# Kernel tuning notes

Hardware: AMD Instinct MI355X
Metric: run time of the kernel (lower is better)

## Reference

```python
import jax, jax.numpy as jnp
import numpy as np

EMBED = 8      # embed_dim == n_qubits == d_k (forced by reshapes in the source)
FFN = 2048
LN_EPS = 1e-5


def _layernorm(x, g, b):
    mu = jnp.mean(x, axis=-1, keepdims=True)
    var = jnp.mean(jnp.square(x - mu), axis=-1, keepdims=True)
    return (x - mu) * jax.lax.rsqrt(var + LN_EPS) * g + b


def _quantum_measure(theta):
    # RX(theta_i) on each wire of |0..0>, CNOT ladder 0->1->...->n-1,
    # then <Z_i>. Closed form: <Z_i> = prod_{j<=i} cos(theta_j).
    return jnp.cumprod(jnp.cos(theta), axis=-1)


def setup_inputs() -> dict:
    key = jax.random.key(0)
    ks = jax.random.split(key, 8)
    B, S = 32, 4096
    s_e = 1.0 / np.sqrt(EMBED)
    s_f = 1.0 / np.sqrt(FFN)
    return {
        "x": jax.random.normal(ks[0], (B, S, EMBED), jnp.float32),
        "Wq": jax.random.uniform(ks[1], (EMBED, EMBED), jnp.float32, -s_e, s_e),
        "Wo": jax.random.uniform(ks[2], (EMBED, EMBED), jnp.float32, -s_e, s_e),
        "W1": jax.random.uniform(ks[3], (FFN, EMBED), jnp.float32, -s_e, s_e),
        "b1": jax.random.uniform(ks[4], (FFN,), jnp.float32, -s_e, s_e),
        "W2": jax.random.uniform(ks[5], (EMBED, FFN), jnp.float32, -s_f, s_f),
        "b2": jax.random.uniform(ks[6], (EMBED,), jnp.float32, -s_f, s_f),
        "g1": jnp.ones((EMBED,), jnp.float32),
        "beta1": jnp.zeros((EMBED,), jnp.float32),
        "g2": jnp.ones((EMBED,), jnp.float32),
        "beta2": jnp.zeros((EMBED,), jnp.float32),
    }


def reference(x, Wq, Wo, W1, b1, W2, b2, g1, beta1, g2, beta2):
    # Quantum multi-head attention (num_heads=1, d_k=n_wires=8).
    # Note: k_proj / v_proj outputs are unused in the original forward.
    q = jnp.einsum("bse,fe->bsf", x, Wq)          # (B,S,E)
    attn = jnp.einsum("bse,fe->bsf", _quantum_measure(q), Wo)
    h = _layernorm(x + attn, g1, beta1)           # dropout is identity (eval)
    # Quantum feed-forward: measure -> linear1 -> relu -> linear2
    m = _quantum_measure(h)                       # (B,S,E)
    hid = jax.nn.relu(jnp.einsum("bse,fe->bsf", m, W1) + b1)  # (B,S,FFN)
    ffn = jnp.einsum("bsf,ef->bse", hid, W2) + b2
    return _layernorm(h + ffn, g2, beta2)
```

## Files before the change

kernel.cpp:

```cpp
#include <hip/hip_runtime.h>
#include <hip/hip_bf16.h>

#define FFN 2048
#define LN_EPS 1e-5f

typedef __attribute__((ext_vector_type(8))) short bf16x8;
typedef __attribute__((ext_vector_type(4))) float f32x4;

union FragU { bf16x8 v; unsigned u[4]; uint4 q; };

static __device__ __forceinline__ unsigned cvtpk(float lo, float hi) {
    unsigned r;
    asm("v_cvt_pk_bf16_f32 %0, %1, %2" : "=v"(r) : "v"(lo), "v"(hi));
    return r;
}

static __device__ __forceinline__ unsigned pkrelu(unsigned a, unsigned z) {
    unsigned r;
    asm("v_pk_max_f16 %0, %1, %2" : "=v"(r) : "v"(a), "v"(z));
    return r;
}

static __device__ __forceinline__ ushort to_bf16(float f) {
    unsigned u = __float_as_uint(f);
    u += 0x7fffu + ((u >> 16) & 1u);
    return (ushort)(u >> 16);
}

__global__ __launch_bounds__(256) void tbq_prep(
    const float* __restrict__ W1, const float* __restrict__ b1,
    const float* __restrict__ W2, uint4* __restrict__ ws)
{
    const int idx = blockIdx.x * 256 + threadIdx.x;
    if (idx >= 6336) return;
    ushort v[8] = {0,0,0,0,0,0,0,0};
    if (idx < 4224) {
        const int rec = idx / 33, r = idx % 33;
        if (r) {
            const int l32 = r - 1, c = l32 & 15, g = l32 >> 4;
            const int s = rec & 1, cc = rec >> 1;
            const int f = cc * 32 + s * 16 + c;
            if (g == 0) {
                #pragma unroll
                for (int j = 0; j < 8; ++j) v[j] = to_bf16(W1[f * 8 + j]);
            } else {
                v[0] = to_bf16(b1[f]);
            }
        }
    } else {
        const int i2 = idx - 4224;
        const int rec = i2 / 33, r = i2 % 33;
        if (r) {
            const int l32 = r - 1, g = l32 >> 3, c = l32 & 7, cc = rec;
            #pragma unroll
            for (int j = 0; j < 8; ++j) {
                const int fl = 4 * g + (j & 3) + 16 * (j >> 2);
                v[j] = to_bf16(W2[c * FFN + cc * 32 + fl]);
            }
        }
    }
    union { ushort s[8]; uint4 q; } pk;
    #pragma unroll
    for (int j = 0; j < 8; ++j) pk.s[j] = v[j];
    ws[idx] = pk.q;
}

__global__ __launch_bounds__(256) void tbq_mfma(
    const float* __restrict__ x,
    const float* __restrict__ Wq,
    const float* __restrict__ Wo,
    const float* __restrict__ b2,
    const float* __restrict__ g1,
    const float* __restrict__ beta1,
    const float* __restrict__ g2,
    const float* __restrict__ beta2,
    const uint4* __restrict__ ws,
    float* __restrict__ out)
{
    __shared__ __align__(16) uint4 mS[128];
    __shared__ __align__(16) float part[4][128][8];

    const int tid  = threadIdx.x;
    const int lane = tid & 63;
    const int wv   = tid >> 6;
    const int c    = lane & 15;
    const int g    = lane >> 4;
    const int tok0 = blockIdx.x * 128;

    const int o1 = (lane < 32) ? (1 + lane) : 0;
    const int o2 = ((lane & 8) == 0) ? (1 + ((lane >> 4) << 3) + (lane & 7)) : 0;

    float h[8];
    if (tid < 128) {
        const int t = tok0 + tid;
        const float4* xr = (const float4*)(x + (size_t)t * 8);
        float4 xa = xr[0], xb = xr[1];
        float xv[8] = {xa.x, xa.y, xa.z, xa.w, xb.x, xb.y, xb.z, xb.w};

        float qm[8];
        {
            float cp = 1.0f;
            #pragma unroll
            for (int f = 0; f < 8; ++f) {
                float acc = 0.0f;
                #pragma unroll
                for (int e = 0; e < 8; ++e) acc += xv[e] * Wq[f * 8 + e];
                cp *= __cosf(acc);
                qm[f] = cp;
            }
        }
        float mu = 0.0f;
        #pragma unroll
        for (int f = 0; f < 8; ++f) {
            float acc = 0.0f;
            #pragma unroll
            for (int e = 0; e < 8; ++e) acc += qm[e] * Wo[f * 8 + e];
            h[f] = xv[f] + acc;
            mu += h[f];
        }
        mu *= 0.125f;
        float var = 0.0f;
        #pragma unroll
        for (int i = 0; i < 8; ++i) { float d = h[i] - mu; var += d * d; }
        var *= 0.125f;
        float rs = rsqrtf(var + LN_EPS);
        #pragma unroll
        for (int i = 0; i < 8; ++i) h[i] = (h[i] - mu) * rs * g1[i] + beta1[i];

        float m[8];
        {
            float cp = 1.0f;
            #pragma unroll
            for (int i = 0; i < 8; ++i) { cp *= __cosf(h[i]); m[i] = cp; }
        }
        uint4 mq;
        mq.x = cvtpk(m[0], m[1]); mq.y = cvtpk(m[2], m[3]);
        mq.z = cvtpk(m[4], m[5]); mq.w = cvtpk(m[6], m[7]);
        mS[tid] = mq;
    }
    __syncthreads();

    FragU B1[8];
    #pragma unroll
    for (int T = 0; T < 8; ++T) {
        uint4 mr = mS[T * 16 + c];
        B1[T].u[0] = (g == 0) ? mr.x : ((g == 1) ? 0x00003F80u : 0u);
        B1[T].u[1] = (g == 0) ? mr.y : 0u;
        B1[T].u[2] = (g == 0) ? mr.z : 0u;
        B1[T].u[3] = (g == 0) ? mr.w : 0u;
    }

    f32x4 z4 = {0.f, 0.f, 0.f, 0.f};
    asm volatile("" : "+v"(z4));
    unsigned zz = 0u;
    asm volatile("" : "+v"(zz));

    f32x4 acc[8] = {{0,0,0,0},{0,0,0,0},{0,0,0,0},{0,0,0,0},
                    {0,0,0,0},{0,0,0,0},{0,0,0,0},{0,0,0,0}};
    const int cc0 = wv * 16;

    #pragma unroll 4
    for (int i = 0; i < 16; ++i) {
        const int cc = cc0 + i;
        const uint4* r0 = ws + cc * 66;
        const uint4* r1 = r0 + 33;
        const uint4* r2 = ws + 4224 + cc * 33;
        FragU F0, F1, A2;
        F0.q = r0[o1];
        F1.q = r1[o1];
        A2.q = r2[o2];

        #pragma unroll
        for (int T = 0; T < 8; ++T) {
            f32x4 c0 = __builtin_amdgcn_mfma_f32_16x16x32_bf16(F0.v, B1[T].v, z4, 0, 0, 0);
            f32x4 c1 = __builtin_amdgcn_mfma_f32_16x16x32_bf16(F1.v, B1[T].v, z4, 0, 0, 0);
            FragU B2;
            B2.u[0] = pkrelu(cvtpk(c0[0], c0[1]), zz);
            B2.u[1] = pkrelu(cvtpk(c0[2], c0[3]), zz);
            B2.u[2] = pkrelu(cvtpk(c1[0], c1[1]), zz);
            B2.u[3] = pkrelu(cvtpk(c1[2], c1[3]), zz);
            acc[T] = __builtin_amdgcn_mfma_f32_16x16x32_bf16(A2.v, B2.v, acc[T], 0, 0, 0);
        }
    }

    if (g < 2) {
        #pragma unroll
        for (int T = 0; T < 8; ++T) {
            *(f32x4*)&part[wv][T * 16 + c][4 * g] = acc[T];
        }
    }
    __syncthreads();

    if (tid < 128) {
        float ffnv[8];
        #pragma unroll
        for (int e = 0; e < 8; ++e)
            ffnv[e] = part[0][tid][e] + part[1][tid][e]
                    + part[2][tid][e] + part[3][tid][e];

        float o[8];
        float mu2 = 0.0f;
        #pragma unroll
        for (int i = 0; i < 8; ++i) { o[i] = h[i] + ffnv[i] + b2[i]; mu2 += o[i]; }
        mu2 *= 0.125f;
        float v2 = 0.0f;
        #pragma unroll
        for (int i = 0; i < 8; ++i) { float d = o[i] - mu2; v2 += d * d; }
        v2 *= 0.125f;
        float rs2 = rsqrtf(v2 + LN_EPS);

        float res[8];
        #pragma unroll
        for (int i = 0; i < 8; ++i) res[i] = (o[i] - mu2) * rs2 * g2[i] + beta2[i];

        float4* orow = (float4*)(out + (size_t)(tok0 + tid) * 8);
        orow[0] = make_float4(res[0], res[1], res[2], res[3]);
        orow[1] = make_float4(res[4], res[5], res[6], res[7]);
    }
}

extern "C" void kernel_launch(void* const* d_in, const int* in_sizes, int n_in,
                              void* d_out, int out_size, void* d_ws, size_t ws_size,
                              hipStream_t stream) {
    const float* x     = (const float*)d_in[0];
    const float* Wq    = (const float*)d_in[1];
    const float* Wo    = (const float*)d_in[2];
    const float* W1    = (const float*)d_in[3];
    const float* b1    = (const float*)d_in[4];
    const float* W2    = (const float*)d_in[5];
    const float* b2    = (const float*)d_in[6];
    const float* g1    = (const float*)d_in[7];
    const float* beta1 = (const float*)d_in[8];
    const float* g2    = (const float*)d_in[9];
    const float* beta2 = (const float*)d_in[10];
    float* out = (float*)d_out;
    uint4* ws = (uint4*)d_ws;

    tbq_prep<<<25, 256, 0, stream>>>(W1, b1, W2, ws);

    const int ntok = in_sizes[0] / 8;
    const int grid = ntok / 128;
    tbq_mfma<<<grid, 256, 0, stream>>>(x, Wq, Wo, b2, g1, beta1, g2, beta2, ws, out);
}
```

Before: 37.80 us.

## Prefetch weight fragments three iterations ahead and raise wave priority around MFMAs

The FFN loop now software-pipelines the weight fragment loads into a 4-slot register ring. The first three chunks are issued before the prologue's attention/LayerNorm math, so those loads overlap with it, and each later load is issued three iterations early. The MFMA block is wrapped in s_setprio raises, and the packed ReLU uses an inline zero constant instead of a zero register. This aims to hide global-load latency on the weights, at the cost of extra VGPRs that may reduce occupancy.

```diff
diff --git a/kernel.cpp b/kernel.cpp
--- a/kernel.cpp
+++ b/kernel.cpp
@@ -15,9 +15,9 @@
     return r;
 }
 
-static __device__ __forceinline__ unsigned pkrelu(unsigned a, unsigned z) {
+static __device__ __forceinline__ unsigned pkrelu(unsigned a) {
     unsigned r;
-    asm("v_pk_max_f16 %0, %1, %2" : "=v"(r) : "v"(a), "v"(z));
+    asm("v_pk_max_f16 %0, %1, 0" : "=v"(r) : "v"(a));
     return r;
 }
 
@@ -90,6 +90,17 @@
     const int o1 = (lane < 32) ? (1 + lane) : 0;
     const int o2 = ((lane & 8) == 0) ? (1 + ((lane >> 4) << 3) + (lane & 7)) : 0;
 
+    const int cc0 = wv * 16;
+
+    FragU F0[4], F1[4], A2[4];
+    #pragma unroll
+    for (int p = 0; p < 3; ++p) {
+        const int cc = cc0 + p;
+        F0[p].q = (ws + cc * 66)[o1];
+        F1[p].q = (ws + cc * 66 + 33)[o1];
+        A2[p].q = (ws + 4224 + cc * 33)[o2];
+    }
+
     float h[8];
     if (tid < 128) {
         const int t = tok0 + tid;
@@ -152,35 +163,33 @@
 
     f32x4 z4 = {0.f, 0.f, 0.f, 0.f};
     asm volatile("" : "+v"(z4));
-    unsigned zz = 0u;
-    asm volatile("" : "+v"(zz));
 
     f32x4 acc[8] = {{0,0,0,0},{0,0,0,0},{0,0,0,0},{0,0,0,0},
                     {0,0,0,0},{0,0,0,0},{0,0,0,0},{0,0,0,0}};
-    const int cc0 = wv * 16;
-
-    #pragma unroll 4
+
+    #pragma unroll
     for (int i = 0; i < 16; ++i) {
-        const int cc = cc0 + i;
-        const uint4* r0 = ws + cc * 66;
-        const uint4* r1 = r0 + 33;
-        const uint4* r2 = ws + 4224 + cc * 33;
-        FragU F0, F1, A2;
-        F0.q = r0[o1];
-        F1.q = r1[o1];
-        A2.q = r2[o2];
-
+        const int cur = i & 3;
+        if (i + 3 < 16) {
+            const int nslot = (i + 3) & 3;
+            const int cc = cc0 + i + 3;
+            F0[nslot].q = (ws + cc * 66)[o1];
+            F1[nslot].q = (ws + cc * 66 + 33)[o1];
+            A2[nslot].q = (ws + 4224 + cc * 33)[o2];
+        }
+        __builtin_amdgcn_s_setprio(1);
         #pragma unroll
         for (int T = 0; T < 8; ++T) {
-            f32x4 c0 = __builtin_amdgcn_mfma_f32_16x16x32_bf16(F0.v, B1[T].v, z4, 0, 0, 0);
-            f32x4 c1 = __builtin_amdgcn_mfma_f32_16x16x32_bf16(F1.v, B1[T].v, z4, 0, 0, 0);
+            f32x4 c0 = __builtin_amdgcn_mfma_f32_16x16x32_bf16(F0[cur].v, B1[T].v, z4, 0, 0, 0);
+            f32x4 c1 = __builtin_amdgcn_mfma_f32_16x16x32_bf16(F1[cur].v, B1[T].v, z4, 0, 0, 0);
             FragU B2;
-            B2.u[0] = pkrelu(cvtpk(c0[0], c0[1]), zz);
-            B2.u[1] = pkrelu(cvtpk(c0[2], c0[3]), zz);
-            B2.u[2] = pkrelu(cvtpk(c1[0], c1[1]), zz);
-            B2.u[3] = pkrelu(cvtpk(c1[2], c1[3]), zz);
-            acc[T] = __builtin_amdgcn_mfma_f32_16x16x32_bf16(A2.v, B2.v, acc[T], 0, 0, 0);
-        }
+            B2.u[0] = pkrelu(cvtpk(c0[0], c0[1]));
+            B2.u[1] = pkrelu(cvtpk(c0[2], c0[3]));
+            B2.u[2] = pkrelu(cvtpk(c1[0], c1[1]));
+            B2.u[3] = pkrelu(cvtpk(c1[2], c1[3]));
+            acc[T] = __builtin_amdgcn_mfma_f32_16x16x32_bf16(A2[cur].v, B2.v, acc[T], 0, 0, 0);
+        }
+        __builtin_amdgcn_s_setprio(0);
     }
 
     if (g < 2) {
```

New measurement: 35.96 us. 4.9% less time.
